# Optimization experiments

Measured on AMD Instinct MI355X. Metric: run time of the kernel, lower is better.

The kernel has to match this reference:

```python
import jax, jax.numpy as jnp
import numpy as np

K_HEADS = 8
D_HEAD = 8
C_IN = 128   # c_x + c_t after channel concat
C_OUT = K_HEADS * D_HEAD  # 64
SMALL = -32767.0  # -2**15 + 1


def setup_inputs() -> dict:
    key = jax.random.key(0)
    ks = jax.random.split(key, 12)
    B, Cx, V, T = 8, 64, 200, 128
    x = jax.random.normal(ks[0], (B, Cx, V, T), dtype=jnp.float32)
    tem_embedding = jax.random.normal(ks[1], (B, Cx, V, T), dtype=jnp.float32)
    s = 0.05
    Wq = jax.random.normal(ks[2], (C_OUT, C_IN), dtype=jnp.float32) * s
    bq = jax.random.normal(ks[3], (C_OUT,), dtype=jnp.float32) * s
    Wk = jax.random.normal(ks[4], (C_OUT, C_IN), dtype=jnp.float32) * s
    bk = jax.random.normal(ks[5], (C_OUT,), dtype=jnp.float32) * s
    Wv = jax.random.normal(ks[6], (C_OUT, C_IN), dtype=jnp.float32) * s
    bv = jax.random.normal(ks[7], (C_OUT,), dtype=jnp.float32) * s
    Wo = jax.random.normal(ks[8], (C_OUT, C_OUT), dtype=jnp.float32) * s
    bo = jax.random.normal(ks[9], (C_OUT,), dtype=jnp.float32) * s
    return {"x": x, "tem_embedding": tem_embedding,
            "Wq": Wq, "bq": bq, "Wk": Wk, "bk": bk,
            "Wv": Wv, "bv": bv, "Wo": Wo, "bo": bo}


def reference(x, tem_embedding, Wq, bq, Wk, bk, Wv, bv, Wo, bo):
    B, _, V, T = x.shape
    # concat temporal embedding on channel dim (last T steps)
    xt = jnp.concatenate([x, tem_embedding[:, :, :, -T:]], axis=1)  # [B, C_IN, V, T]

    def proj(W, b):  # 1x1 conv == channel einsum
        return jnp.einsum('oi,bivt->bovt', W, xt) + b[None, :, None, None]

    def heads(t):  # [B, K*d, V, T] -> [K*B, V, T, d] (split on dim1, cat on dim0)
        t = t.reshape(B, K_HEADS, D_HEAD, V, T)
        t = jnp.transpose(t, (1, 0, 3, 4, 2))  # [K, B, V, T, d]
        return t.reshape(K_HEADS * B, V, T, D_HEAD)

    q = heads(proj(Wq, bq))
    k = heads(proj(Wk, bk))
    v = heads(proj(Wv, bv))

    attn = jnp.einsum('nvtd,nvsd->nvts', q, k) / jnp.sqrt(jnp.float32(D_HEAD))
    causal = jnp.tril(jnp.ones((T, T), dtype=bool))  # [T, T]
    attn = jnp.where(causal[None, None, :, :], attn, SMALL)
    attn = jax.nn.softmax(attn, axis=-1)
    out = jnp.einsum('nvts,nvsd->nvtd', attn, v)  # [K*B, V, T, d]

    # merge heads back: [K*B, V, T, d] -> [B, K*d, V, T]
    out = out.reshape(K_HEADS, B, V, T, D_HEAD)
    out = jnp.transpose(out, (1, 0, 4, 2, 3)).reshape(B, K_HEADS * D_HEAD, V, T)
    out = jnp.einsum('oi,bivt->bovt', Wo, out) + bo[None, :, None, None]
    return jax.nn.relu(out)
```

## Files before the change

### kernel.cpp

```cpp
#include <hip/hip_runtime.h>
#include <stdint.h>

#define TPB 512

constexpr int Bb   = 8;
constexpr int Vv   = 200;
constexpr int Tt   = 128;
constexpr int CIN  = 128;
constexpr int COUT = 64;

typedef __attribute__((ext_vector_type(8))) short bf16x8;
typedef __attribute__((ext_vector_type(4))) short short4v;
typedef __attribute__((ext_vector_type(4))) float f32x4;

__device__ __forceinline__ unsigned short f2bf(float f) {
    union { float f; unsigned u; } x; x.f = f;
    unsigned r = x.u + 0x7fffu + ((x.u >> 16) & 1u);
    return (unsigned short)(r >> 16);
}
__device__ __forceinline__ unsigned pk2(float a, float b) {
    return (unsigned)f2bf(a) | ((unsigned)f2bf(b) << 16);
}

#if __has_builtin(__builtin_amdgcn_mfma_f32_16x16x16bf16_1k)
#define MFMA16(a, b, c) __builtin_amdgcn_mfma_f32_16x16x16bf16_1k(a, b, c, 0, 0, 0)
#else
__device__ __forceinline__ f32x4 mfma16_asm(short4v a, short4v b, f32x4 c) {
    f32x4 d;
    asm("v_mfma_f32_16x16x16_bf16 %0, %1, %2, %3" : "=v"(d) : "v"(a), "v"(b), "v"(c));
    return d;
}
#define MFMA16(a, b, c) mfma16_asm(a, b, c)
#endif

__global__ void prep_w(const float* __restrict__ Wq, const float* __restrict__ Wk,
                       const float* __restrict__ Wv, const float* __restrict__ Wo,
                       unsigned short* __restrict__ ws) {
    int i = blockIdx.x * 256 + threadIdx.x;
    float v;
    if (i < 8192)       v = Wq[i];
    else if (i < 16384) v = Wk[i - 8192];
    else if (i < 24576) v = Wv[i - 16384];
    else                v = Wo[i - 24576];
    ws[i] = f2bf(v);
}

__global__ __launch_bounds__(TPB, 4)
void tatt_fused(const float* __restrict__ x, const float* __restrict__ tem,
                const float* __restrict__ bq, const float* __restrict__ bk,
                const float* __restrict__ bv, const float* __restrict__ bo,
                const unsigned short* __restrict__ ws,
                float* __restrict__ out)
{
    __shared__ __align__(16) unsigned char smem[65536];
    unsigned short* qk = (unsigned short*)smem;
    unsigned short* vt = (unsigned short*)(smem + 32768);
    unsigned short* xt = (unsigned short*)(smem + 49152);
    unsigned short* ot = (unsigned short*)(smem + 49152);

    const int tid = threadIdx.x;
    const int w = tid >> 6, lane = tid & 63;
    const int l15 = lane & 15, qd = lane >> 4;
    const int b = blockIdx.x / Vv, v = blockIdx.x % Vv;
    const float QS = 1.44269504088896f * 0.35355339059327f;

    const float* bpa[3] = {bq, bk, bv};

    for (int half = 0; half < 2; ++half) {
        __syncthreads();
        #pragma unroll
        for (int k = 0; k < 4; ++k) {
            int idx = tid + k * TPB;
            int c = idx & 127, t4 = idx >> 7;
            const float* src = (c < 64 ? x : tem)
                + ((b * 64 + (c & 63)) * Vv + v) * Tt + half * 64 + t4 * 4;
            float4 f = *(const float4*)src;
            float fv[4] = {f.x, f.y, f.z, f.w};
            #pragma unroll
            for (int j = 0; j < 4; ++j) {
                int t = t4 * 4 + j;
                xt[t * CIN + (((c >> 3) ^ (t & 15)) << 3) + (c & 7)] = f2bf(fv[j]);
            }
        }
        __syncthreads();
        #pragma unroll
        for (int j = 0; j < 6; ++j) {
            int tile = w * 6 + j;
            int p = tile >> 4, rem = tile & 15;
            int ot_ = rem & 3, tt = rem >> 2;
            f32x4 acc = {0.f, 0.f, 0.f, 0.f};
            const unsigned short* Wb  = ws + p * 8192 + (ot_ * 16 + l15) * CIN + qd * 8;
            const unsigned short* Bbp = xt + (tt * 16 + l15) * CIN;
            #pragma unroll
            for (int kc = 0; kc < 4; ++kc) {
                bf16x8 a = *(const bf16x8*)(Wb + kc * 32);
                int phys = (kc * 4 + qd) ^ l15;
                bf16x8 bbv = *(const bf16x8*)(Bbp + phys * 8);
                acc = __builtin_amdgcn_mfma_f32_16x16x32_bf16(a, bbv, acc, 0, 0, 0);
            }
            int obase = ot_ * 16 + qd * 4;
            float4 bias = *(const float4*)(bpa[p] + obase);
            float bb4[4] = {bias.x, bias.y, bias.z, bias.w};
            int tg = half * 64 + tt * 16 + l15;
            if (p == 2) {
                #pragma unroll
                for (int r = 0; r < 4; ++r) {
                    int dg = obase + r;
                    int tp = tg ^ ((((dg >> 2) & 3)) << 4);
                    vt[dg * 128 + tp] = f2bf(acc[r] + bb4[r]);
                }
            } else {
                float sc = (p == 0) ? QS : 1.0f;
                ushort4 st4;
                st4.x = f2bf((acc[0] + bb4[0]) * sc);
                st4.y = f2bf((acc[1] + bb4[1]) * sc);
                st4.z = f2bf((acc[2] + bb4[2]) * sc);
                st4.w = f2bf((acc[3] + bb4[3]) * sc);
                int phys = (obase >> 2) ^ (tg & 14);
                *(ushort4*)(qk + p * 8192 + tg * 64 + phys * 4) = st4;
            }
        }
    }
    __syncthreads();

    {
        const int h = w;
        short4v vfrag[8];
        {
            int dg = h * 8 + l15;
            int swz = ((dg >> 2) & 3) << 4;
            #pragma unroll
            for (int st = 0; st < 8; ++st) {
                short4v f = {0, 0, 0, 0};
                if (l15 < 8) {
                    int sp = (st * 16 + qd * 4) ^ swz;
                    f = *(const short4v*)(vt + dg * 128 + sp);
                }
                vfrag[st] = f;
            }
        }
        bool dmask[4];
        #pragma unroll
        for (int r = 0; r < 4; ++r) dmask[r] = (qd * 4 + r) <= l15;
        const int qkoff = ((h * 2) ^ (l15 & 14)) << 2;

        for (int tt = 0; tt < 8; ++tt) {
            bf16x8 qf = {0, 0, 0, 0, 0, 0, 0, 0};
            if (qd == 0) qf = *(const bf16x8*)(qk + (tt * 16 + l15) * 64 + qkoff);
            f32x4 o0 = {0.f, 0.f, 0.f, 0.f}, o1 = {0.f, 0.f, 0.f, 0.f};
            float lac = 0.f;
            #pragma unroll
            for (int st = 0; st < 8; ++st) {
                if (st <= tt) {
                    bf16x8 kf = {0, 0, 0, 0, 0, 0, 0, 0};
                    if (qd == 0) kf = *(const bf16x8*)(qk + 8192 + (st * 16 + l15) * 64 + qkoff);
                    f32x4 z = {0.f, 0.f, 0.f, 0.f};
                    f32x4 s = __builtin_amdgcn_mfma_f32_16x16x32_bf16(kf, qf, z, 0, 0, 0);
                    float p0 = __builtin_amdgcn_exp2f(s[0]);
                    float p1 = __builtin_amdgcn_exp2f(s[1]);
                    float p2 = __builtin_amdgcn_exp2f(s[2]);
                    float p3 = __builtin_amdgcn_exp2f(s[3]);
                    if (st == tt) {
                        p0 = dmask[0] ? p0 : 0.f;
                        p1 = dmask[1] ? p1 : 0.f;
                        p2 = dmask[2] ? p2 : 0.f;
                        p3 = dmask[3] ? p3 : 0.f;
                    }
                    lac += (p0 + p1) + (p2 + p3);
                    int pp0 = (int)pk2(p0, p1), pp1 = (int)pk2(p2, p3);
                    short4v pf;
                    pf[0] = (short)(pp0 & 0xffff); pf[1] = (short)(pp0 >> 16);
                    pf[2] = (short)(pp1 & 0xffff); pf[3] = (short)(pp1 >> 16);
                    if (st & 1) o1 = MFMA16(vfrag[st], pf, o1);
                    else        o0 = MFMA16(vfrag[st], pf, o0);
                }
            }
            float l = lac;
            l += __shfl_xor(l, 16, 64);
            l += __shfl_xor(l, 32, 64);
            float rl = __builtin_amdgcn_rcpf(l);
            if (qd < 2) {
                float r0 = (o0[0] + o1[0]) * rl, r1 = (o0[1] + o1[1]) * rl;
                float r2 = (o0[2] + o1[2]) * rl, r3 = (o0[3] + o1[3]) * rl;
                int t = tt * 16 + l15;
                uint2 st2;
                st2.x = pk2(r0, r1);
                st2.y = pk2(r2, r3);
                *(uint2*)(ot + t * 64 + (((h * 2 + qd) ^ (l15 & 14)) << 2)) = st2;
            }
        }
    }
    __syncthreads();

    {
        const int tt = w;
        #pragma unroll
        for (int ot_ = 0; ot_ < 4; ++ot_) {
            f32x4 acc = {0.f, 0.f, 0.f, 0.f};
            const unsigned short* Ab = ws + 24576 + (ot_ * 16 + l15) * COUT + qd * 8;
            #pragma unroll
            for (int kc = 0; kc < 2; ++kc) {
                bf16x8 a = *(const bf16x8*)(Ab + kc * 32);
                bf16x8 bbv = *(const bf16x8*)(ot + (tt * 16 + l15) * 64
                                 + (((kc * 8 + qd * 2) ^ (l15 & 14)) << 2));
                acc = __builtin_amdgcn_mfma_f32_16x16x32_bf16(a, bbv, acc, 0, 0, 0);
            }
            int obase = ot_ * 16 + qd * 4;
            float4 bias = *(const float4*)(bo + obase);
            float bb4[4] = {bias.x, bias.y, bias.z, bias.w};
            int t = tt * 16 + l15;
            #pragma unroll
            for (int r = 0; r < 4; ++r) {
                float val = acc[r] + bb4[r];
                out[((b * COUT + obase + r) * Vv + v) * Tt + t] = val > 0.f ? val : 0.f;
            }
        }
    }
}

extern "C" void kernel_launch(void* const* d_in, const int* in_sizes, int n_in,
                              void* d_out, int out_size, void* d_ws, size_t ws_size,
                              hipStream_t stream) {
    (void)in_sizes; (void)n_in; (void)ws_size; (void)out_size;
    const float* x   = (const float*)d_in[0];
    const float* tem = (const float*)d_in[1];
    const float* Wq  = (const float*)d_in[2];
    const float* bq  = (const float*)d_in[3];
    const float* Wk  = (const float*)d_in[4];
    const float* bk  = (const float*)d_in[5];
    const float* Wv  = (const float*)d_in[6];
    const float* bv  = (const float*)d_in[7];
    const float* Wo  = (const float*)d_in[8];
    const float* bo  = (const float*)d_in[9];
    float* out = (float*)d_out;
    unsigned short* ws = (unsigned short*)d_ws;

    prep_w<<<dim3(112), dim3(256), 0, stream>>>(Wq, Wk, Wv, Wo, ws);
    tatt_fused<<<dim3(Bb * Vv), dim3(TPB), 0, stream>>>(
        x, tem, bq, bk, bv, bo, ws, out);
}
```

Before: 269.1 us.

## Pre-swizzle bf16 weights into MFMA fragment order and hoist K fragments

The weight prep kernel now stores the bf16 weights in per-lane MFMA fragment order, so each lane loads its A fragment as one contiguous 16-byte chunk and a wave's fragment load is fully coalesced instead of strided across rows. The input staging is remapped so each thread handles one channel across a contiguous run of time steps, which shortens the address arithmetic. K fragments for attention are loaded into registers once per head rather than once per query tile. This raises register pressure under the launch bound of 4 blocks of 512 threads.

```diff
diff --git a/kernel.cpp b/kernel.cpp
--- a/kernel.cpp
+++ b/kernel.cpp
@@ -37,12 +37,23 @@
                        const float* __restrict__ Wv, const float* __restrict__ Wo,
                        unsigned short* __restrict__ ws) {
     int i = blockIdx.x * 256 + threadIdx.x;
-    float v;
-    if (i < 8192)       v = Wq[i];
-    else if (i < 16384) v = Wk[i - 8192];
-    else if (i < 24576) v = Wv[i - 16384];
-    else                v = Wo[i - 24576];
-    ws[i] = f2bf(v);
+    if (i < 24576) {
+        int f = i >> 9, r = i & 511;
+        int l = r >> 3, e = r & 7;
+        int p = f >> 4, ot_ = (f >> 2) & 3, kc = f & 3;
+        int row = ot_ * 16 + (l & 15);
+        int col = kc * 32 + (l >> 4) * 8 + e;
+        const float* W = (p == 0) ? Wq : ((p == 1) ? Wk : Wv);
+        ws[i] = f2bf(W[row * 128 + col]);
+    } else {
+        int i2 = i - 24576;
+        int f = i2 >> 9, r = i2 & 511;
+        int l = r >> 3, e = r & 7;
+        int ot_ = f >> 1, kc = f & 1;
+        int row = ot_ * 16 + (l & 15);
+        int col = kc * 32 + (l >> 4) * 8 + e;
+        ws[i] = f2bf(Wo[row * 64 + col]);
+    }
 }
 
 __global__ __launch_bounds__(TPB, 4)
@@ -64,22 +75,19 @@
     const int b = blockIdx.x / Vv, v = blockIdx.x % Vv;
     const float QS = 1.44269504088896f * 0.35355339059327f;
 
-    const float* bpa[3] = {bq, bk, bv};
+    const int cS = tid >> 2, tqS = tid & 3;
+    const float* srcBase = (cS < 64 ? x : tem) + ((long)(b * 64 + (cS & 63)) * Vv + v) * Tt;
 
     for (int half = 0; half < 2; ++half) {
         __syncthreads();
         #pragma unroll
         for (int k = 0; k < 4; ++k) {
-            int idx = tid + k * TPB;
-            int c = idx & 127, t4 = idx >> 7;
-            const float* src = (c < 64 ? x : tem)
-                + ((b * 64 + (c & 63)) * Vv + v) * Tt + half * 64 + t4 * 4;
-            float4 f = *(const float4*)src;
+            float4 f = *(const float4*)(srcBase + half * 64 + k * 16 + tqS * 4);
             float fv[4] = {f.x, f.y, f.z, f.w};
             #pragma unroll
             for (int j = 0; j < 4; ++j) {
-                int t = t4 * 4 + j;
-                xt[t * CIN + (((c >> 3) ^ (t & 15)) << 3) + (c & 7)] = f2bf(fv[j]);
+                int t = k * 16 + tqS * 4 + j;
+                xt[t * CIN + (((cS >> 3) ^ (t & 15)) << 3) + (cS & 7)] = f2bf(fv[j]);
             }
         }
         __syncthreads();
@@ -88,18 +96,19 @@
             int tile = w * 6 + j;
             int p = tile >> 4, rem = tile & 15;
             int ot_ = rem & 3, tt = rem >> 2;
+            int cmb = p * 4 + ot_;
             f32x4 acc = {0.f, 0.f, 0.f, 0.f};
-            const unsigned short* Wb  = ws + p * 8192 + (ot_ * 16 + l15) * CIN + qd * 8;
             const unsigned short* Bbp = xt + (tt * 16 + l15) * CIN;
             #pragma unroll
             for (int kc = 0; kc < 4; ++kc) {
-                bf16x8 a = *(const bf16x8*)(Wb + kc * 32);
+                bf16x8 a = *(const bf16x8*)(ws + (cmb * 4 + kc) * 512 + lane * 8);
                 int phys = (kc * 4 + qd) ^ l15;
                 bf16x8 bbv = *(const bf16x8*)(Bbp + phys * 8);
                 acc = __builtin_amdgcn_mfma_f32_16x16x32_bf16(a, bbv, acc, 0, 0, 0);
             }
             int obase = ot_ * 16 + qd * 4;
-            float4 bias = *(const float4*)(bpa[p] + obase);
+            const float* bp_ = (p == 0) ? bq : ((p == 1) ? bk : bv);
+            float4 bias = *(const float4*)(bp_ + obase);
             float bb4[4] = {bias.x, bias.y, bias.z, bias.w};
             int tg = half * 64 + tt * 16 + l15;
             if (p == 2) {
@@ -139,10 +148,17 @@
                 vfrag[st] = f;
             }
         }
+        const int qkoff = ((h * 2) ^ (l15 & 14)) << 2;
+        bf16x8 kfr[8];
+        #pragma unroll
+        for (int st = 0; st < 8; ++st) {
+            bf16x8 kf = {0, 0, 0, 0, 0, 0, 0, 0};
+            if (qd == 0) kf = *(const bf16x8*)(qk + 8192 + (st * 16 + l15) * 64 + qkoff);
+            kfr[st] = kf;
+        }
         bool dmask[4];
         #pragma unroll
         for (int r = 0; r < 4; ++r) dmask[r] = (qd * 4 + r) <= l15;
-        const int qkoff = ((h * 2) ^ (l15 & 14)) << 2;
 
         for (int tt = 0; tt < 8; ++tt) {
             bf16x8 qf = {0, 0, 0, 0, 0, 0, 0, 0};
@@ -152,10 +168,8 @@
             #pragma unroll
             for (int st = 0; st < 8; ++st) {
                 if (st <= tt) {
-                    bf16x8 kf = {0, 0, 0, 0, 0, 0, 0, 0};
-                    if (qd == 0) kf = *(const bf16x8*)(qk + 8192 + (st * 16 + l15) * 64 + qkoff);
                     f32x4 z = {0.f, 0.f, 0.f, 0.f};
-                    f32x4 s = __builtin_amdgcn_mfma_f32_16x16x32_bf16(kf, qf, z, 0, 0, 0);
+                    f32x4 s = __builtin_amdgcn_mfma_f32_16x16x32_bf16(kfr[st], qf, z, 0, 0, 0);
                     float p0 = __builtin_amdgcn_exp2f(s[0]);
                     float p1 = __builtin_amdgcn_exp2f(s[1]);
                     float p2 = __builtin_amdgcn_exp2f(s[2]);
@@ -197,10 +211,9 @@
         #pragma unroll
         for (int ot_ = 0; ot_ < 4; ++ot_) {
             f32x4 acc = {0.f, 0.f, 0.f, 0.f};
-            const unsigned short* Ab = ws + 24576 + (ot_ * 16 + l15) * COUT + qd * 8;
             #pragma unroll
             for (int kc = 0; kc < 2; ++kc) {
-                bf16x8 a = *(const bf16x8*)(Ab + kc * 32);
+                bf16x8 a = *(const bf16x8*)(ws + 24576 + (ot_ * 2 + kc) * 512 + lane * 8);
                 bf16x8 bbv = *(const bf16x8*)(ot + (tt * 16 + l15) * 64
                                  + (((kc * 8 + qd * 2) ^ (l15 & 14)) << 2));
                 acc = __builtin_amdgcn_mfma_f32_16x16x32_bf16(a, bbv, acc, 0, 0, 0);
@@ -212,7 +225,7 @@
             #pragma unroll
             for (int r = 0; r < 4; ++r) {
                 float val = acc[r] + bb4[r];
-                out[((b * COUT + obase + r) * Vv + v) * Tt + t] = val > 0.f ? val : 0.f;
+                out[((long)(b * COUT + obase + r) * Vv + v) * Tt + t] = val > 0.f ? val : 0.f;
             }
         }
     }
```

Result: slower. 303.3 us (+12.7%).
